# Kernel tuning notes

Measured on AMD Instinct MI355X. Metric: run time of the kernel, lower is better.

The kernel has to match this reference:

```python
import jax, jax.numpy as jnp
import numpy as np

HIDDEN = 1024
NUM_EXPERTS = 8
TOP_K = 2
INNER = HIDDEN * 2
B, S = 4, 2048


def setup_inputs() -> dict:
    key = jax.random.key(0)
    ks = jax.random.split(key, 8)
    sd = 1.0 / np.sqrt(HIDDEN)
    si = 1.0 / np.sqrt(INNER)
    return {
        "x": jax.random.normal(ks[0], (B, S, HIDDEN), dtype=jnp.float32),
        "Wr": jax.random.uniform(ks[1], (HIDDEN, NUM_EXPERTS), jnp.float32, -sd, sd),
        "br": jax.random.uniform(ks[2], (NUM_EXPERTS,), jnp.float32, -sd, sd),
        "W1": jax.random.uniform(ks[3], (NUM_EXPERTS, HIDDEN, INNER), jnp.float32, -sd, sd),
        "b1": jax.random.uniform(ks[4], (NUM_EXPERTS, INNER), jnp.float32, -sd, sd),
        "W2": jax.random.uniform(ks[5], (NUM_EXPERTS, INNER, HIDDEN), jnp.float32, -si, si),
        "b2": jax.random.uniform(ks[6], (NUM_EXPERTS, HIDDEN), jnp.float32, -si, si),
    }


def reference(x, Wr, br, W1, b1, W2, b2):
    batch, seq, hidden = x.shape
    tokens = x.reshape(-1, hidden)                       # [N, d]
    n = tokens.shape[0]
    logits = tokens @ Wr + br                            # [N, E]
    top_w, top_i = jax.lax.top_k(logits, TOP_K)          # [N, k]
    top_w = jax.nn.softmax(top_w, axis=-1)
    # Dense per-token expert weights (zero outside top-k) — equivalent to the
    # sorted-dispatch + index_add combine in the original.
    weights = jnp.zeros((n, NUM_EXPERTS), dtype=top_w.dtype)
    weights = weights.at[jnp.arange(n)[:, None], top_i].add(top_w)  # [N, E]
    out = jnp.zeros_like(tokens)
    for e in range(NUM_EXPERTS):  # fixed small loop over experts
        h = jax.nn.relu(tokens @ W1[e] + b1[e])          # [N, inner]
        y = h @ W2[e] + b2[e]                            # [N, d]
        out = out + y * weights[:, e:e + 1]
    return out.reshape(batch, seq, hidden)
```

## Files before the change

### kernel.cpp

```cpp
#include <hip/hip_runtime.h>
#include <stdint.h>

#define HID    1024
#define EXPERTS 8
#define TOPK   2
#define INNER  2048
#define NTOK   8192
#define NPAIR  (NTOK * TOPK)
#define MAXT   136
#define BM 128
#define BN 128
#define BK 32
#define AFFS  17
#define NSLOT 200

typedef _Float16 f16;
typedef f16   f16x8 __attribute__((ext_vector_type(8)));
typedef float f32x4 __attribute__((ext_vector_type(4)));

#define VMCNT(n) asm volatile("s_waitcnt vmcnt(" #n ")" ::: "memory")
#define BARRIER() do { __builtin_amdgcn_s_barrier(); asm volatile("" ::: "memory"); } while (0)

__device__ __forceinline__ void gload_lds16(const void* g, void* l) {
  __builtin_amdgcn_global_load_lds(
      (const __attribute__((address_space(1))) void*)g,
      (__attribute__((address_space(3))) void*)l, 16, 0, 0);
}

__global__ void router_kernel(const float* __restrict__ x,
                              const float* __restrict__ Wr,
                              const float* __restrict__ br,
                              int* __restrict__ e_sel, float* __restrict__ w_sel) {
  int gid  = blockIdx.x * blockDim.x + threadIdx.x;
  int wid  = gid >> 6;
  int lane = gid & 63;
  if (wid >= NTOK) return;

  const f32x4* xr = (const f32x4*)(x + (size_t)wid * HID);
  float acc[EXPERTS];
#pragma unroll
  for (int e = 0; e < EXPERTS; ++e) acc[e] = 0.f;
#pragma unroll
  for (int j = 0; j < HID / 256; ++j) {
    f32x4 xv = xr[j * 64 + lane];
    int   k  = (j * 64 + lane) * 4;
    const float* wr = Wr + (size_t)k * EXPERTS;
#pragma unroll
    for (int r = 0; r < 4; ++r) {
      float xs = xv[r];
      f32x4 w0 = *(const f32x4*)(wr + r * 8);
      f32x4 w1 = *(const f32x4*)(wr + r * 8 + 4);
#pragma unroll
      for (int e = 0; e < 4; ++e) { acc[e] += xs * w0[e]; acc[4 + e] += xs * w1[e]; }
    }
  }
#pragma unroll
  for (int e = 0; e < EXPERTS; ++e) {
#pragma unroll
    for (int off = 32; off > 0; off >>= 1) acc[e] += __shfl_xor(acc[e], off);
  }
  if (lane == 0) {
    float lg[EXPERTS];
#pragma unroll
    for (int e = 0; e < EXPERTS; ++e) lg[e] = acc[e] + br[e];
    int e0 = 0; float l0 = lg[0];
#pragma unroll
    for (int e = 1; e < EXPERTS; ++e) if (lg[e] > l0) { l0 = lg[e]; e0 = e; }
    int e1 = -1; float l1 = -3.4e38f;
#pragma unroll
    for (int e = 0; e < EXPERTS; ++e) if (e != e0 && lg[e] > l1) { l1 = lg[e]; e1 = e; }
    float a  = __expf(l1 - l0);
    float w0 = 1.f / (1.f + a);
    float w1 = a * w0;
    e_sel[wid * 2]     = e0;  e_sel[wid * 2 + 1] = e1;
    w_sel[wid * 2]     = w0;  w_sel[wid * 2 + 1] = w1;
  }
}

__global__ __launch_bounds__(1024) void dispatch_kernel(
    const int* __restrict__ e_sel, const float* __restrict__ w_sel,
    int* __restrict__ tok_list, float* __restrict__ wt_list,
    int* __restrict__ counts, int* __restrict__ bases,
    int* __restrict__ slot_e, int* __restrict__ slot_m0,
    int* __restrict__ slot_g, int* __restrict__ tinfo) {
  __shared__ int scnt[EXPERTS][1024];
  __shared__ int etot[EXPERTS];
  __shared__ int ebase[EXPERTS];
  int tid = threadIdx.x, lane = tid & 63, wv = tid >> 6;

  int myE[16]; float myW[16];
  int lc[EXPERTS];
#pragma unroll
  for (int e = 0; e < EXPERTS; ++e) lc[e] = 0;
#pragma unroll
  for (int i = 0; i < 16; ++i) {
    int p = tid * 16 + i;
    myE[i] = e_sel[p];
    myW[i] = w_sel[p];
#pragma unroll
    for (int e = 0; e < EXPERTS; ++e) lc[e] += (myE[i] == e);
  }
#pragma unroll
  for (int e = 0; e < EXPERTS; ++e) scnt[e][tid] = lc[e];
  __syncthreads();

  if (wv < EXPERTS) {
    int run = 0;
    for (int c = 0; c < 16; ++c) {
      int v = scnt[wv][c * 64 + lane];
      int incl = v;
#pragma unroll
      for (int off = 1; off < 64; off <<= 1) {
        int n = __shfl_up(incl, off);
        if (lane >= off) incl += n;
      }
      scnt[wv][c * 64 + lane] = run + incl - v;
      run += __shfl(incl, 63);
    }
    if (lane == 0) etot[wv] = run;
  }
  __syncthreads();

  if (tid < NSLOT) slot_e[tid] = -1;
  __syncthreads();
  if (tid == 0) {
    int s = 0;
    for (int e = 0; e < EXPERTS; ++e) {
      ebase[e] = s; bases[e] = s; counts[e] = etot[e]; s += etot[e];
    }
    int ov = AFFS * EXPERTS, gt = 0;
    for (int e = 0; e < EXPERTS; ++e) {
      int ntl = (etot[e] + BM - 1) / BM;
      for (int i = 0; i < ntl; ++i) {
        int sl = (i < AFFS) ? (e + EXPERTS * i) : (ov++);
        slot_e[sl] = e; slot_m0[sl] = i * BM; slot_g[sl] = gt++;
      }
    }
    tinfo[0] = gt;
  }
  __syncthreads();

  int cur[EXPERTS];
#pragma unroll
  for (int e = 0; e < EXPERTS; ++e) cur[e] = ebase[e] + scnt[e][tid];
#pragma unroll
  for (int i = 0; i < 16; ++i) {
    int p = 0;
#pragma unroll
    for (int e = 0; e < EXPERTS; ++e) if (myE[i] == e) p = cur[e]++;
    tok_list[p] = (tid * 16 + i) >> 1;
    wt_list[p]  = myW[i];
  }
}

__global__ void convert_x_kernel(const float* __restrict__ x,
                                 f16* __restrict__ x16, int n8) {
  int i = blockIdx.x * blockDim.x + threadIdx.x;
  int stride = gridDim.x * blockDim.x;
  for (; i < n8; i += stride) {
    f32x4 a = ((const f32x4*)x)[i * 2];
    f32x4 b = ((const f32x4*)x)[i * 2 + 1];
    f16x8 o;
#pragma unroll
    for (int j = 0; j < 4; ++j) { o[j] = (f16)a[j]; o[4 + j] = (f16)b[j]; }
    ((f16x8*)x16)[i] = o;
  }
}

__global__ void transpose_cvt_kernel(const float* __restrict__ src,
                                     f16* __restrict__ dst, int R, int C) {
  __shared__ float tile[32][33];
  int z = blockIdx.z;
  src += (size_t)z * R * C;
  dst += (size_t)z * R * C;
  int c0 = blockIdx.x * 32, r0 = blockIdx.y * 32;
  int tx = threadIdx.x, ty = threadIdx.y;
#pragma unroll
  for (int i = 0; i < 4; ++i)
    tile[ty + i * 8][tx] = src[(size_t)(r0 + ty + i * 8) * C + c0 + tx];
  __syncthreads();
#pragma unroll
  for (int i = 0; i < 4; ++i)
    dst[(size_t)(c0 + ty + i * 8) * R + r0 + tx] = (f16)tile[tx][ty + i * 8];
}


#define STAGE4(BUF) do {                                                      \
  _Pragma("unroll") for (int i_ = 0; i_ < 2; ++i_) {                          \
    gload_lds16(gA[i_], (BUF) + i_ * 2048 + wid * 512); gA[i_] += BK;         \
    gload_lds16(gB[i_], (BUF) + 4096 + i_ * 2048 + wid * 512); gB[i_] += BK;  \
  }                                                                           \
} while (0)

#define COMPUTE8(BUF) do {                                                    \
  f16x8 af_[4], bf_[4];                                                       \
  _Pragma("unroll") for (int mi_ = 0; mi_ < 4; ++mi_)                         \
    af_[mi_] = *(const f16x8*)((BUF) + (wm + mi_ * 16 + ar) * 32 + cswz * 8); \
  _Pragma("unroll") for (int ni_ = 0; ni_ < 4; ++ni_)                         \
    bf_[ni_] = *(const f16x8*)((BUF) + 4096 +                                 \
                               (wn + ni_ * 16 + ar) * 32 + cswz * 8);         \
  _Pragma("unroll") for (int mi_ = 0; mi_ < 4; ++mi_)                         \
    _Pragma("unroll") for (int ni_ = 0; ni_ < 4; ++ni_)                       \
      acc[mi_][ni_] = __builtin_amdgcn_mfma_f32_16x16x32_f16(                 \
          af_[mi_], bf_[ni_], acc[mi_][ni_], 0, 0, 0);                        \
} while (0)

#define PIPELINE_LOOP(NT) do {                                                \
  STAGE4(q0); STAGE4(q1);                                                     \
  VMCNT(4); BARRIER();                                                        \
  for (int t = 0; t < (NT); ++t) {                                            \
    if (t + 2 < (NT)) { STAGE4(q2); }                                         \
    COMPUTE8(q0);                                                             \
    if (t + 2 < (NT)) { VMCNT(4); } else { VMCNT(0); }                        \
    BARRIER();                                                                \
    f16* tm_ = q0; q0 = q1; q1 = q2; q2 = tm_;                                \
  }                                                                           \
} while (0)

__global__ __launch_bounds__(256, 3) void gemm1_kernel(
    const f16* __restrict__ x16, const f16* __restrict__ w1t,
    const float* __restrict__ bias1, const int* __restrict__ tok_list,
    const int* __restrict__ counts, const int* __restrict__ bases,
    const int* __restrict__ slot_e, const int* __restrict__ slot_m0,
    const int* __restrict__ slot_g, int c0, int G,
    f16* __restrict__ h16) {
  int sx = blockIdx.x;
  int e  = slot_e[sx];
  if (e < 0) return;
  int g  = slot_g[sx];
  if (g < c0 || g >= c0 + G) return;
  int m0 = slot_m0[sx];
  int cnt = counts[e], base = bases[e];
  int n0 = blockIdx.y * BN;
  const f16* Bg = w1t + (size_t)e * INNER * HID;

  __shared__ __align__(16) f16 LDS[3 * 8192];
  f16 *q0 = LDS, *q1 = LDS + 8192, *q2 = LDS + 2 * 8192;

  int tid = threadIdx.x, lane = tid & 63, wid = tid >> 6;
  int wm = (wid >> 1) * 64, wn = (wid & 1) * 64;
  int ar = lane & 15, hi = lane >> 4;
  int cswz = hi ^ ((ar >> 1) & 3);

  int trow = tid >> 2;
  int gcol = (tid & 3) ^ ((tid >> 3) & 3);
  const f16* gA[2];
  const f16* gB[2];
#pragma unroll
  for (int i = 0; i < 2; ++i) {
    int row = i * 64 + trow;
    int tok = tok_list[base + min(m0 + row, cnt - 1)];
    gA[i] = x16 + (size_t)tok * HID + gcol * 8;
    gB[i] = Bg + (size_t)(n0 + row) * HID + gcol * 8;
  }

  f32x4 acc[4][4];
#pragma unroll
  for (int i = 0; i < 4; ++i)
#pragma unroll
    for (int j = 0; j < 4; ++j) acc[i][j] = (f32x4){0.f, 0.f, 0.f, 0.f};

  PIPELINE_LOOP(HID / BK);

  int colc = ar, rbase = hi * 4;
  float bb[4];
#pragma unroll
  for (int ni = 0; ni < 4; ++ni)
    bb[ni] = bias1[(size_t)e * INNER + n0 + wn + ni * 16 + colc];
#pragma unroll
  for (int mi = 0; mi < 4; ++mi)
#pragma unroll
    for (int r = 0; r < 4; ++r) {
      int ml = wm + mi * 16 + rbase + r;
      if (m0 + ml < cnt) {
        size_t rowoff = (size_t)((g - c0) * BM + ml) * INNER + n0 + wn + colc;
#pragma unroll
        for (int ni = 0; ni < 4; ++ni) {
          float v = acc[mi][ni][r] + bb[ni];
          h16[rowoff + ni * 16] = (f16)fmaxf(v, 0.f);
        }
      }
    }
}

__global__ __launch_bounds__(256, 3) void gemm2_kernel(
    const f16* __restrict__ h16, const f16* __restrict__ w2t,
    const float* __restrict__ bias2, const int* __restrict__ tok_list,
    const float* __restrict__ wt_list, const int* __restrict__ counts,
    const int* __restrict__ bases,
    const int* __restrict__ slot_e, const int* __restrict__ slot_m0,
    const int* __restrict__ slot_g, int c0, int G,
    float* __restrict__ out) {
  int sx = blockIdx.x;
  int e  = slot_e[sx];
  if (e < 0) return;
  int g  = slot_g[sx];
  if (g < c0 || g >= c0 + G) return;
  int m0 = slot_m0[sx];
  int cnt = counts[e], base = bases[e];
  int d0 = blockIdx.y * BN;
  int kc = blockIdx.z;
  int koff = kc * (INNER / 2);
  const f16* Bg = w2t + (size_t)e * HID * INNER;

  __shared__ __align__(16) f16 LDS[3 * 8192];
  f16 *q0 = LDS, *q1 = LDS + 8192, *q2 = LDS + 2 * 8192;

  int tid = threadIdx.x, lane = tid & 63, wid = tid >> 6;
  int wm = (wid >> 1) * 64, wn = (wid & 1) * 64;
  int ar = lane & 15, hi = lane >> 4;
  int cswz = hi ^ ((ar >> 1) & 3);

  int trow = tid >> 2;
  int gcol = (tid & 3) ^ ((tid >> 3) & 3);
  const f16* gA[2];
  const f16* gB[2];
#pragma unroll
  for (int i = 0; i < 2; ++i) {
    int row  = i * 64 + trow;
    int lrow = min(m0 + row, cnt - 1) - m0;
    gA[i] = h16 + ((size_t)(g - c0) * BM + lrow) * INNER + koff + gcol * 8;
    gB[i] = Bg + (size_t)(d0 + row) * INNER + koff + gcol * 8;
  }

  f32x4 acc[4][4];
#pragma unroll
  for (int i = 0; i < 4; ++i)
#pragma unroll
    for (int j = 0; j < 4; ++j) acc[i][j] = (f32x4){0.f, 0.f, 0.f, 0.f};

  PIPELINE_LOOP((INNER / 2) / BK);

  int colc = ar, rbase = hi * 4;
  float bb[4];
#pragma unroll
  for (int ni = 0; ni < 4; ++ni)
    bb[ni] = (kc == 0) ? bias2[(size_t)e * HID + d0 + wn + ni * 16 + colc] : 0.f;
#pragma unroll
  for (int mi = 0; mi < 4; ++mi)
#pragma unroll
    for (int r = 0; r < 4; ++r) {
      int ml = wm + mi * 16 + rbase + r;
      if (m0 + ml < cnt) {
        int   p   = base + m0 + ml;
        int   tok = tok_list[p];
        float w   = wt_list[p];
        float* orow = out + (size_t)tok * HID + d0 + wn + colc;
#pragma unroll
        for (int ni = 0; ni < 4; ++ni) {
          float v = acc[mi][ni][r] + bb[ni];
          atomicAdd(orow + ni * 16, v * w);
        }
      }
    }
}

extern "C" void kernel_launch(void* const* d_in, const int* in_sizes, int n_in,
                              void* d_out, int out_size, void* d_ws, size_t ws_size,
                              hipStream_t stream) {
  (void)in_sizes; (void)n_in;
  const float* x  = (const float*)d_in[0];
  const float* Wr = (const float*)d_in[1];
  const float* br = (const float*)d_in[2];
  const float* W1 = (const float*)d_in[3];
  const float* b1 = (const float*)d_in[4];
  const float* W2 = (const float*)d_in[5];
  const float* b2 = (const float*)d_in[6];
  float* out = (float*)d_out;

  char*  ws  = (char*)d_ws;
  size_t off = 0;
  auto alloc = [&](size_t bytes) {
    char* p = ws + off;
    off += bytes; off = (off + 255) & ~(size_t)255;
    return p;
  };
  int*   tok_list = (int*)alloc(NPAIR * sizeof(int));
  float* wt_list  = (float*)alloc(NPAIR * sizeof(float));
  int*   e_sel    = (int*)alloc(NTOK * 2 * sizeof(int));
  float* w_sel    = (float*)alloc(NTOK * 2 * sizeof(float));
  int*   counts   = (int*)alloc(EXPERTS * sizeof(int));
  int*   bases    = (int*)alloc(EXPERTS * sizeof(int));
  int*   slot_e   = (int*)alloc(NSLOT * sizeof(int));
  int*   slot_m0  = (int*)alloc(NSLOT * sizeof(int));
  int*   slot_g   = (int*)alloc(NSLOT * sizeof(int));
  int*   tinfo    = (int*)alloc(16 * sizeof(int));
  f16*   w1t      = (f16*)alloc((size_t)EXPERTS * HID * INNER * sizeof(f16));
  f16*   w2t      = (f16*)alloc((size_t)EXPERTS * HID * INNER * sizeof(f16));
  f16*   x16      = (f16*)alloc((size_t)NTOK * HID * sizeof(f16));
  const size_t TILE_BYTES = (size_t)BM * INNER * sizeof(f16);
  size_t rem = (ws_size > off) ? (ws_size - off) : 0;
  int G = (int)(rem / TILE_BYTES);
  if (G < 1) G = 1;
  if (G > MAXT) G = MAXT;
  int nch = (MAXT + G - 1) / G;
  f16* h16 = (f16*)(ws + off);

  hipMemsetAsync(out, 0, (size_t)out_size * sizeof(float), stream);

  convert_x_kernel<<<2048, 256, 0, stream>>>(x, x16, NTOK * HID / 8);
  transpose_cvt_kernel<<<dim3(INNER / 32, HID / 32, EXPERTS), dim3(32, 8), 0, stream>>>(
      W1, w1t, HID, INNER);
  transpose_cvt_kernel<<<dim3(HID / 32, INNER / 32, EXPERTS), dim3(32, 8), 0, stream>>>(
      W2, w2t, INNER, HID);
  router_kernel<<<NTOK / 4, 256, 0, stream>>>(x, Wr, br, e_sel, w_sel);
  dispatch_kernel<<<1, 1024, 0, stream>>>(e_sel, w_sel, tok_list, wt_list,
                                          counts, bases, slot_e, slot_m0, slot_g, tinfo);

  for (int c = 0; c < nch; ++c) {
    int c0 = c * G;
    gemm1_kernel<<<dim3(NSLOT, INNER / BN, 1), 256, 0, stream>>>(
        x16, w1t, b1, tok_list, counts, bases, slot_e, slot_m0, slot_g, c0, G, h16);
    gemm2_kernel<<<dim3(NSLOT, HID / BN, 2), 256, 0, stream>>>(
        h16, w2t, b2, tok_list, wt_list, counts, bases, slot_e, slot_m0, slot_g, c0, G, out);
  }
}
```

Baseline: 502.7 us.

## Use 256-row tiles with 512-thread blocks, drop gemm2 split-K, fuse x conversion into router

The M tile doubles to 256 rows and blocks grow to 512 threads (8 waves), so each B (weight) tile staged in LDS is shared by twice as many token rows. This cuts weight traffic per token and the number of slots. gemm2 no longer splits K in two, which halves the fp32 atomic adds to the output, at the cost of less parallelism. The fp32-to-fp16 conversion of x moves into the router kernel, removing a separate pass over x. LDS use per block grows to 72KB, so fewer blocks can be resident per CU.

```diff
diff --git a/kernel.cpp b/kernel.cpp
--- a/kernel.cpp
+++ b/kernel.cpp
@@ -7,12 +7,12 @@
 #define INNER  2048
 #define NTOK   8192
 #define NPAIR  (NTOK * TOPK)
-#define MAXT   136
-#define BM 128
+#define MAXT   72
+#define BM 256
 #define BN 128
 #define BK 32
-#define AFFS  17
-#define NSLOT 200
+#define AFFS  9
+#define NSLOT 144
 
 typedef _Float16 f16;
 typedef f16   f16x8 __attribute__((ext_vector_type(8)));
@@ -30,19 +30,26 @@
 __global__ void router_kernel(const float* __restrict__ x,
                               const float* __restrict__ Wr,
                               const float* __restrict__ br,
-                              int* __restrict__ e_sel, float* __restrict__ w_sel) {
+                              int* __restrict__ e_sel, float* __restrict__ w_sel,
+                              f16* __restrict__ x16) {
   int gid  = blockIdx.x * blockDim.x + threadIdx.x;
   int wid  = gid >> 6;
   int lane = gid & 63;
   if (wid >= NTOK) return;
 
   const f32x4* xr = (const f32x4*)(x + (size_t)wid * HID);
+  f16* xw = x16 + (size_t)wid * HID;
   float acc[EXPERTS];
 #pragma unroll
   for (int e = 0; e < EXPERTS; ++e) acc[e] = 0.f;
 #pragma unroll
   for (int j = 0; j < HID / 256; ++j) {
     f32x4 xv = xr[j * 64 + lane];
+    union { f16 h[4]; double d; } cv;
+#pragma unroll
+    for (int r = 0; r < 4; ++r) cv.h[r] = (f16)xv[r];
+    *(double*)(xw + (j * 64 + lane) * 4) = cv.d;
+
     int   k  = (j * 64 + lane) * 4;
     const float* wr = Wr + (size_t)k * EXPERTS;
 #pragma unroll
@@ -153,20 +160,6 @@
   }
 }
 
-__global__ void convert_x_kernel(const float* __restrict__ x,
-                                 f16* __restrict__ x16, int n8) {
-  int i = blockIdx.x * blockDim.x + threadIdx.x;
-  int stride = gridDim.x * blockDim.x;
-  for (; i < n8; i += stride) {
-    f32x4 a = ((const f32x4*)x)[i * 2];
-    f32x4 b = ((const f32x4*)x)[i * 2 + 1];
-    f16x8 o;
-#pragma unroll
-    for (int j = 0; j < 4; ++j) { o[j] = (f16)a[j]; o[4 + j] = (f16)b[j]; }
-    ((f16x8*)x16)[i] = o;
-  }
-}
-
 __global__ void transpose_cvt_kernel(const float* __restrict__ src,
                                      f16* __restrict__ dst, int R, int C) {
   __shared__ float tile[32][33];
@@ -185,19 +178,20 @@
 }
 
 
-#define STAGE4(BUF) do {                                                      \
-  _Pragma("unroll") for (int i_ = 0; i_ < 2; ++i_) {                          \
-    gload_lds16(gA[i_], (BUF) + i_ * 2048 + wid * 512); gA[i_] += BK;         \
-    gload_lds16(gB[i_], (BUF) + 4096 + i_ * 2048 + wid * 512); gB[i_] += BK;  \
-  }                                                                           \
+#define BUFSZ 12288
+
+#define STAGE3(BUF) do {                                                      \
+  gload_lds16(gA[0], (BUF) + wid * 512);          gA[0] += BK;                \
+  gload_lds16(gA[1], (BUF) + 4096 + wid * 512);   gA[1] += BK;                \
+  gload_lds16(gB0,   (BUF) + 8192 + wid * 512);   gB0   += BK;                \
 } while (0)
 
-#define COMPUTE8(BUF) do {                                                    \
+#define COMPUTE16(BUF) do {                                                   \
   f16x8 af_[4], bf_[4];                                                       \
   _Pragma("unroll") for (int mi_ = 0; mi_ < 4; ++mi_)                         \
     af_[mi_] = *(const f16x8*)((BUF) + (wm + mi_ * 16 + ar) * 32 + cswz * 8); \
   _Pragma("unroll") for (int ni_ = 0; ni_ < 4; ++ni_)                         \
-    bf_[ni_] = *(const f16x8*)((BUF) + 4096 +                                 \
+    bf_[ni_] = *(const f16x8*)((BUF) + 8192 +                                 \
                                (wn + ni_ * 16 + ar) * 32 + cswz * 8);         \
   _Pragma("unroll") for (int mi_ = 0; mi_ < 4; ++mi_)                         \
     _Pragma("unroll") for (int ni_ = 0; ni_ < 4; ++ni_)                       \
@@ -206,18 +200,18 @@
 } while (0)
 
 #define PIPELINE_LOOP(NT) do {                                                \
-  STAGE4(q0); STAGE4(q1);                                                     \
-  VMCNT(4); BARRIER();                                                        \
+  STAGE3(q0); STAGE3(q1);                                                     \
+  VMCNT(3); BARRIER();                                                        \
   for (int t = 0; t < (NT); ++t) {                                            \
-    if (t + 2 < (NT)) { STAGE4(q2); }                                         \
-    COMPUTE8(q0);                                                             \
-    if (t + 2 < (NT)) { VMCNT(4); } else { VMCNT(0); }                        \
+    if (t + 2 < (NT)) { STAGE3(q2); }                                         \
+    COMPUTE16(q0);                                                            \
+    if (t + 2 < (NT)) { VMCNT(3); } else { VMCNT(0); }                        \
     BARRIER();                                                                \
     f16* tm_ = q0; q0 = q1; q1 = q2; q2 = tm_;                                \
   }                                                                           \
 } while (0)
 
-__global__ __launch_bounds__(256, 3) void gemm1_kernel(
+__global__ __launch_bounds__(512, 4) void gemm1_kernel(
     const f16* __restrict__ x16, const f16* __restrict__ w1t,
     const float* __restrict__ bias1, const int* __restrict__ tok_list,
     const int* __restrict__ counts, const int* __restrict__ bases,
@@ -234,8 +228,8 @@
   int n0 = blockIdx.y * BN;
   const f16* Bg = w1t + (size_t)e * INNER * HID;
 
-  __shared__ __align__(16) f16 LDS[3 * 8192];
-  f16 *q0 = LDS, *q1 = LDS + 8192, *q2 = LDS + 2 * 8192;
+  __shared__ __align__(16) f16 LDS[3 * BUFSZ];
+  f16 *q0 = LDS, *q1 = LDS + BUFSZ, *q2 = LDS + 2 * BUFSZ;
 
   int tid = threadIdx.x, lane = tid & 63, wid = tid >> 6;
   int wm = (wid >> 1) * 64, wn = (wid & 1) * 64;
@@ -244,15 +238,12 @@
 
   int trow = tid >> 2;
   int gcol = (tid & 3) ^ ((tid >> 3) & 3);
+  int tok0 = tok_list[base + min(m0 + trow, cnt - 1)];
+  int tok1 = tok_list[base + min(m0 + 128 + trow, cnt - 1)];
   const f16* gA[2];
-  const f16* gB[2];
-#pragma unroll
-  for (int i = 0; i < 2; ++i) {
-    int row = i * 64 + trow;
-    int tok = tok_list[base + min(m0 + row, cnt - 1)];
-    gA[i] = x16 + (size_t)tok * HID + gcol * 8;
-    gB[i] = Bg + (size_t)(n0 + row) * HID + gcol * 8;
-  }
+  gA[0] = x16 + (size_t)tok0 * HID + gcol * 8;
+  gA[1] = x16 + (size_t)tok1 * HID + gcol * 8;
+  const f16* gB0 = Bg + (size_t)(n0 + trow) * HID + gcol * 8;
 
   f32x4 acc[4][4];
 #pragma unroll
@@ -283,7 +274,7 @@
     }
 }
 
-__global__ __launch_bounds__(256, 3) void gemm2_kernel(
+__global__ __launch_bounds__(512, 4) void gemm2_kernel(
     const f16* __restrict__ h16, const f16* __restrict__ w2t,
     const float* __restrict__ bias2, const int* __restrict__ tok_list,
     const float* __restrict__ wt_list, const int* __restrict__ counts,
@@ -299,12 +290,10 @@
   int m0 = slot_m0[sx];
   int cnt = counts[e], base = bases[e];
   int d0 = blockIdx.y * BN;
-  int kc = blockIdx.z;
-  int koff = kc * (INNER / 2);
   const f16* Bg = w2t + (size_t)e * HID * INNER;
 
-  __shared__ __align__(16) f16 LDS[3 * 8192];
-  f16 *q0 = LDS, *q1 = LDS + 8192, *q2 = LDS + 2 * 8192;
+  __shared__ __align__(16) f16 LDS[3 * BUFSZ];
+  f16 *q0 = LDS, *q1 = LDS + BUFSZ, *q2 = LDS + 2 * BUFSZ;
 
   int tid = threadIdx.x, lane = tid & 63, wid = tid >> 6;
   int wm = (wid >> 1) * 64, wn = (wid & 1) * 64;
@@ -313,15 +302,12 @@
 
   int trow = tid >> 2;
   int gcol = (tid & 3) ^ ((tid >> 3) & 3);
+  int lrow0 = min(m0 + trow, cnt - 1) - m0;
+  int lrow1 = min(m0 + 128 + trow, cnt - 1) - m0;
   const f16* gA[2];
-  const f16* gB[2];
-#pragma unroll
-  for (int i = 0; i < 2; ++i) {
-    int row  = i * 64 + trow;
-    int lrow = min(m0 + row, cnt - 1) - m0;
-    gA[i] = h16 + ((size_t)(g - c0) * BM + lrow) * INNER + koff + gcol * 8;
-    gB[i] = Bg + (size_t)(d0 + row) * INNER + koff + gcol * 8;
-  }
+  gA[0] = h16 + ((size_t)(g - c0) * BM + lrow0) * INNER + gcol * 8;
+  gA[1] = h16 + ((size_t)(g - c0) * BM + lrow1) * INNER + gcol * 8;
+  const f16* gB0 = Bg + (size_t)(d0 + trow) * INNER + gcol * 8;
 
   f32x4 acc[4][4];
 #pragma unroll
@@ -329,13 +315,13 @@
 #pragma unroll
     for (int j = 0; j < 4; ++j) acc[i][j] = (f32x4){0.f, 0.f, 0.f, 0.f};
 
-  PIPELINE_LOOP((INNER / 2) / BK);
+  PIPELINE_LOOP(INNER / BK);
 
   int colc = ar, rbase = hi * 4;
   float bb[4];
 #pragma unroll
   for (int ni = 0; ni < 4; ++ni)
-    bb[ni] = (kc == 0) ? bias2[(size_t)e * HID + d0 + wn + ni * 16 + colc] : 0.f;
+    bb[ni] = bias2[(size_t)e * HID + d0 + wn + ni * 16 + colc];
 #pragma unroll
   for (int mi = 0; mi < 4; ++mi)
 #pragma unroll
@@ -398,20 +384,19 @@
 
   hipMemsetAsync(out, 0, (size_t)out_size * sizeof(float), stream);
 
-  convert_x_kernel<<<2048, 256, 0, stream>>>(x, x16, NTOK * HID / 8);
+  router_kernel<<<NTOK / 4, 256, 0, stream>>>(x, Wr, br, e_sel, w_sel, x16);
   transpose_cvt_kernel<<<dim3(INNER / 32, HID / 32, EXPERTS), dim3(32, 8), 0, stream>>>(
       W1, w1t, HID, INNER);
   transpose_cvt_kernel<<<dim3(HID / 32, INNER / 32, EXPERTS), dim3(32, 8), 0, stream>>>(
       W2, w2t, INNER, HID);
-  router_kernel<<<NTOK / 4, 256, 0, stream>>>(x, Wr, br, e_sel, w_sel);
   dispatch_kernel<<<1, 1024, 0, stream>>>(e_sel, w_sel, tok_list, wt_list,
                                           counts, bases, slot_e, slot_m0, slot_g, tinfo);
 
   for (int c = 0; c < nch; ++c) {
     int c0 = c * G;
-    gemm1_kernel<<<dim3(NSLOT, INNER / BN, 1), 256, 0, stream>>>(
+    gemm1_kernel<<<dim3(NSLOT, INNER / BN, 1), 512, 0, stream>>>(
         x16, w1t, b1, tok_list, counts, bases, slot_e, slot_m0, slot_g, c0, G, h16);
-    gemm2_kernel<<<dim3(NSLOT, HID / BN, 2), 256, 0, stream>>>(
+    gemm2_kernel<<<dim3(NSLOT, HID / BN, 1), 512, 0, stream>>>(
         h16, w2t, b2, tok_list, wt_list, counts, bases, slot_e, slot_m0, slot_g, c0, G, out);
   }
 }
```

Measured after the change: 485.1 us. 3.5% less time.
